# Kernel tuning notes

Hardware: AMD Instinct MI355X
Metric: run time of the kernel (lower is better)

The kernel has to match this reference:

```python
import jax, jax.numpy as jnp
import numpy as np
from jax import lax

DIL_R = 2            # dilation_radius
K = 2 * DIL_R + 1    # 5x5 morphology kernel
FOCAL_ALPHA = 0.25
FOCAL_GAMMA = 2.0
BOUNDARY_W = 1.0
IGNORE_IDX = 250


def setup_inputs() -> dict:
    key = jax.random.key(0)
    k1, k2 = jax.random.split(key)
    pred = jax.random.normal(k1, (32, 2, 512, 512), dtype=jnp.float32)
    target = jax.random.randint(k2, (32, 512, 512), 0, 2, dtype=jnp.int64)
    return {"pred": pred, "target": target}


def _boundary_mask(target):
    # labels float, 5x5 all-ones conv with 'same' padding (zero pad),
    # dilated = (conv > 0), eroded = (-conv(-x) > K*K-1) == (conv(x) > K*K-1)
    x = target.astype(jnp.float32)[:, None]                    # [B,1,H,W]
    kern = jnp.ones((1, 1, K, K), dtype=jnp.float32)
    s = lax.conv_general_dilated(x, kern, (1, 1), 'SAME',
                                 dimension_numbers=('NCHW', 'OIHW', 'NCHW'))
    dilated = (s > 0).astype(jnp.float32)
    eroded = (s > (K * K - 1)).astype(jnp.float32)
    return (dilated - eroded)[:, 0]                            # [B,H,W]


def _loss(pred, target, boundary):
    logp = jax.nn.log_softmax(pred, axis=1)                    # [B,2,H,W]
    # per-pixel CE
    ce_pix = -jnp.take_along_axis(logp, target[:, None].astype(jnp.int32), axis=1)[:, 0]  # [B,H,W]
    # main CE with ignore_index=250
    valid = (target != IGNORE_IDX)
    ce_loss = jnp.sum(ce_pix * valid) / jnp.maximum(jnp.sum(valid), 1)
    # focal loss (no ignore, mean over all pixels)
    pt = jnp.exp(-ce_pix)
    focal = jnp.mean(FOCAL_ALPHA * (1.0 - pt) ** FOCAL_GAMMA * ce_pix)
    # boundary dice on class-1 prob
    prob1 = jnp.exp(logp[:, 1])                                # softmax(pred,1)[:,1]
    tgt_f = target.astype(jnp.float32)
    bp = prob1 * boundary
    bt = tgt_f * boundary
    inter = jnp.sum(bp * bt, axis=(1, 2))
    union = jnp.sum(bp, axis=(1, 2)) + jnp.sum(bt, axis=(1, 2))
    dice = 2.0 * inter / (union + 1e-8)
    bdice = 1.0 - jnp.mean(dice)
    return ce_loss + BOUNDARY_W * focal + BOUNDARY_W * bdice


def reference(pred, target):
    boundary = _boundary_mask(target)
    return _loss(pred, target, boundary)
```

## Files before the change

kernel.cpp:

```cpp
#include <hip/hip_runtime.h>
#include <math.h>

#define BATCH 32
#define HH 512
#define WW 512
#define TH 16
#define HALO 2
#define SRH (TH + 2*HALO)
#define NDW (WW / 4)
#define CSTRIDE 132
#define NPIX ((float)BATCH * HH * WW)
#define HW (HH * WW)
#define NBLK (BATCH * (HH / TH))


__global__ __launch_bounds__(256, 4) void bel_main_kernel(
        const float* __restrict__ pred,
        const int*   __restrict__ target,
        float*       __restrict__ ws) {
    __shared__ unsigned int t8[SRH][NDW];
    __shared__ unsigned int csum[TH][CSTRIDE];
    __shared__ float red[6][4];

    const int tid = threadIdx.x;
    const int bid = blockIdx.x;
    const int b   = bid >> 5;
    const int ty  = bid & 31;
    const int y0  = ty * TH;
    const size_t tb = (size_t)b * HW;

    if (tid < 2 * TH) {
        int rr = tid >> 1;
        csum[rr][(tid & 1) ? (NDW + 1) : 0] = 0u;
    }

    #pragma unroll
    for (int it = 0; it < (SRH * NDW) / 256; ++it) {
        const int i  = tid + 256 * it;
        const int r  = i >> 7;
        const int c4 = i & 127;
        const int gy = y0 - HALO + r;
        unsigned int packed = 0u;
        if ((unsigned)gy < (unsigned)HH) {
            const int4 v = *(const int4*)(target + tb + ((size_t)gy << 9) + (c4 << 2));
            packed = (unsigned)v.x | ((unsigned)v.y << 8)
                   | ((unsigned)v.z << 16) | ((unsigned)v.w << 24);
        }
        t8[r][c4] = packed;
    }
    __syncthreads();

    #pragma unroll
    for (int it = 0; it < (TH * NDW) / 256; ++it) {
        const int j = tid + 256 * it;
        const int r = j >> 7;
        const int c = j & 127;
        csum[r][c + 1] = t8[r][c] + t8[r+1][c] + t8[r+2][c]
                       + t8[r+3][c] + t8[r+4][c];
    }
    __syncthreads();

    const float4* __restrict__ pr0 = (const float4*)(pred + tb * 2);
    const float4* __restrict__ pr1 = (const float4*)(pred + tb * 2 + HW);
    const int base4 = (y0 << 7) + tid;

    float4 F0[8], F1[8];
    #pragma unroll
    for (int it = 0; it < 8; ++it) F0[it] = pr0[base4 + 256 * it];
    #pragma unroll
    for (int it = 0; it < 8; ++it) F1[it] = pr1[base4 + 256 * it];

    float ce_acc = 0.f, cnt_acc = 0.f, focal_acc = 0.f;
    float inter_acc = 0.f, bp_acc = 0.f, bt_acc = 0.f;

    const unsigned long long M5 = 0xFFFFFFFFFFull;
    const unsigned long long ALL5 = 0x0505050505ull;

    const int g  = tid & 127;
    const int rb = tid >> 7;

    #pragma unroll
    for (int it = 0; it < 8; ++it) {
        const int r = rb + 2 * it;

        const float4 f0 = F0[it];
        const float4 f1 = F1[it];

        const unsigned int L = csum[r][g];
        const unsigned int M = csum[r][g + 1];
        const unsigned int R = csum[r][g + 2];
        const unsigned int tdw = t8[r + HALO][g];

        const unsigned long long lo  = (unsigned long long)L | ((unsigned long long)M << 32);
        const unsigned long long mid = (unsigned long long)M | ((unsigned long long)R << 32);

        #pragma unroll
        for (int i = 0; i < 4; ++i) {
            unsigned long long w;
            if      (i == 0) w = (lo  >> 16) & M5;
            else if (i == 1) w = (lo  >> 24) & M5;
            else if (i == 2) w =  mid        & M5;
            else             w = (mid >>  8) & M5;
            const float bm = (w != 0ull && w != ALL5) ? 1.0f : 0.0f;

            const unsigned int tv = (tdw >> (8 * i)) & 0xFFu;

            const float p0 = (i == 0) ? f0.x : (i == 1) ? f0.y : (i == 2) ? f0.z : f0.w;
            const float p1 = (i == 0) ? f1.x : (i == 1) ? f1.y : (i == 2) ? f1.z : f1.w;

            const float d  = p1 - p0;
            const float e  = __expf(-fabsf(d));
            const float rz = 1.0f / (1.0f + e);
            const float pmin = e * rz;
            const float prob1 = (d >= 0.0f) ? rz : pmin;
            const float pt = tv ? prob1 : (1.0f - prob1);
            const float ce = -__logf(pt);

            const float valid = (tv != 250u) ? 1.0f : 0.0f;
            ce_acc  += ce * valid;
            cnt_acc += valid;

            const float omp = 1.0f - pt;
            focal_acc += omp * omp * ce;

            const float bp = prob1 * bm;
            const float bt = (float)tv * bm;
            inter_acc += bp * bt;
            bp_acc    += bp;
            bt_acc    += bt;
        }
    }

    float vals[6] = {ce_acc, cnt_acc, focal_acc * 0.25f, inter_acc, bp_acc, bt_acc};
    #pragma unroll
    for (int jj = 0; jj < 6; ++jj) {
        float v = vals[jj];
        #pragma unroll
        for (int off = 32; off > 0; off >>= 1)
            v += __shfl_down(v, off, 64);
        vals[jj] = v;
    }
    const int wave = tid >> 6;
    const int lane = tid & 63;
    if (lane == 0) {
        #pragma unroll
        for (int jj = 0; jj < 6; ++jj) red[jj][wave] = vals[jj];
    }
    __syncthreads();
    if (tid == 0) {
        float* p = ws + bid * 8;
        #pragma unroll
        for (int jj = 0; jj < 6; ++jj)
            p[jj] = red[jj][0] + red[jj][1] + red[jj][2] + red[jj][3];
    }
}

__global__ void bel_finalize_kernel(const float* __restrict__ ws,
                                    float* __restrict__ out) {
    __shared__ float simg[BATCH][4];
    const int t = threadIdx.x;
    const int b = t >> 3;
    const int s = t & 7;

    float a0 = 0.f, a1 = 0.f, a2 = 0.f, a3 = 0.f, a4 = 0.f, a5 = 0.f;
    #pragma unroll
    for (int k = 0; k < 4; ++k) {
        const int bid = (b << 5) + s + (k << 3);
        const float* p = ws + bid * 8;
        a0 += p[0]; a1 += p[1]; a2 += p[2];
        a3 += p[3]; a4 += p[4]; a5 += p[5];
    }
    #pragma unroll
    for (int off = 4; off > 0; off >>= 1) {
        a0 += __shfl_down(a0, off, 8);
        a1 += __shfl_down(a1, off, 8);
        a2 += __shfl_down(a2, off, 8);
        a3 += __shfl_down(a3, off, 8);
        a4 += __shfl_down(a4, off, 8);
        a5 += __shfl_down(a5, off, 8);
    }
    if (s == 0) {
        simg[b][0] = a0;
        simg[b][1] = a1;
        simg[b][2] = a2;
        simg[b][3] = 2.0f * a3 / (a4 + a5 + 1e-8f);
    }
    __syncthreads();
    if (t < BATCH) {
        float ce  = simg[t][0];
        float cnt = simg[t][1];
        float foc = simg[t][2];
        float dc  = simg[t][3];
        #pragma unroll
        for (int off = 16; off > 0; off >>= 1) {
            ce  += __shfl_down(ce,  off, 32);
            cnt += __shfl_down(cnt, off, 32);
            foc += __shfl_down(foc, off, 32);
            dc  += __shfl_down(dc,  off, 32);
        }
        if (t == 0) {
            const float ce_loss = ce / fmaxf(cnt, 1.0f);
            const float focal   = foc / NPIX;
            const float bdice   = 1.0f - dc / (float)BATCH;
            out[0] = ce_loss + focal + bdice;
        }
    }
}

extern "C" void kernel_launch(void* const* d_in, const int* in_sizes, int n_in,
                              void* d_out, int out_size, void* d_ws, size_t ws_size,
                              hipStream_t stream) {
    const float* pred   = (const float*)d_in[0];
    const int*   target = (const int*)d_in[1];
    float* ws  = (float*)d_ws;
    float* out = (float*)d_out;

    bel_main_kernel<<<NBLK, 256, 0, stream>>>(pred, target, ws);
    bel_finalize_kernel<<<1, 256, 0, stream>>>(ws, out);
}
```

Baseline: 116.7 us.

## Split fused kernel into boundary-mask and loss kernels with finer grid

Splits the fused kernel in two. The first kernel computes the 5x5 boundary mask from the target labels and writes it as packed bytes to workspace. The second kernel streams pred, target and the mask across a finer grid of 2048 blocks to accumulate the loss partials. This drops the shared-memory staging and register-heavy preloading from the loss pass, which may raise occupancy, but it re-reads target, writes and reads an extra 8 MB mask, and adds a kernel launch.

```diff
diff --git a/kernel.cpp b/kernel.cpp
--- a/kernel.cpp
+++ b/kernel.cpp
@@ -11,16 +11,20 @@
 #define CSTRIDE 132
 #define NPIX ((float)BATCH * HH * WW)
 #define HW (HH * WW)
-#define NBLK (BATCH * (HH / TH))
-
-
-__global__ __launch_bounds__(256, 4) void bel_main_kernel(
-        const float* __restrict__ pred,
-        const int*   __restrict__ target,
-        float*       __restrict__ ws) {
+#define HW4 (HW / 4)
+#define NBLK_A (BATCH * (HH / TH))
+#define SEGS 64
+#define NBLK_B (BATCH * SEGS)
+#define NSTG ((SRH * NDW) / 256)
+#define NCS  ((TH * NDW) / 256)
+
+#define PARTIALS_FLOATS (NBLK_B * 8)
+
+__global__ __launch_bounds__(256) void boundary_kernel(
+        const int* __restrict__ target,
+        unsigned int* __restrict__ bmask) {
     __shared__ unsigned int t8[SRH][NDW];
     __shared__ unsigned int csum[TH][CSTRIDE];
-    __shared__ float red[6][4];
 
     const int tid = threadIdx.x;
     const int bid = blockIdx.x;
@@ -35,7 +39,7 @@
     }
 
     #pragma unroll
-    for (int it = 0; it < (SRH * NDW) / 256; ++it) {
+    for (int it = 0; it < NSTG; ++it) {
         const int i  = tid + 256 * it;
         const int r  = i >> 7;
         const int c4 = i & 127;
@@ -51,7 +55,7 @@
     __syncthreads();
 
     #pragma unroll
-    for (int it = 0; it < (TH * NDW) / 256; ++it) {
+    for (int it = 0; it < NCS; ++it) {
         const int j = tid + 256 * it;
         const int r = j >> 7;
         const int c = j & 127;
@@ -60,40 +64,23 @@
     }
     __syncthreads();
 
-    const float4* __restrict__ pr0 = (const float4*)(pred + tb * 2);
-    const float4* __restrict__ pr1 = (const float4*)(pred + tb * 2 + HW);
-    const int base4 = (y0 << 7) + tid;
-
-    float4 F0[8], F1[8];
-    #pragma unroll
-    for (int it = 0; it < 8; ++it) F0[it] = pr0[base4 + 256 * it];
-    #pragma unroll
-    for (int it = 0; it < 8; ++it) F1[it] = pr1[base4 + 256 * it];
-
-    float ce_acc = 0.f, cnt_acc = 0.f, focal_acc = 0.f;
-    float inter_acc = 0.f, bp_acc = 0.f, bt_acc = 0.f;
-
     const unsigned long long M5 = 0xFFFFFFFFFFull;
     const unsigned long long ALL5 = 0x0505050505ull;
-
     const int g  = tid & 127;
     const int rb = tid >> 7;
 
     #pragma unroll
     for (int it = 0; it < 8; ++it) {
         const int r = rb + 2 * it;
-
-        const float4 f0 = F0[it];
-        const float4 f1 = F1[it];
+        const int y = y0 + r;
 
         const unsigned int L = csum[r][g];
         const unsigned int M = csum[r][g + 1];
         const unsigned int R = csum[r][g + 2];
-        const unsigned int tdw = t8[r + HALO][g];
-
         const unsigned long long lo  = (unsigned long long)L | ((unsigned long long)M << 32);
         const unsigned long long mid = (unsigned long long)M | ((unsigned long long)R << 32);
 
+        unsigned int packed = 0u;
         #pragma unroll
         for (int i = 0; i < 4; ++i) {
             unsigned long long w;
@@ -101,22 +88,58 @@
             else if (i == 1) w = (lo  >> 24) & M5;
             else if (i == 2) w =  mid        & M5;
             else             w = (mid >>  8) & M5;
-            const float bm = (w != 0ull && w != ALL5) ? 1.0f : 0.0f;
-
-            const unsigned int tv = (tdw >> (8 * i)) & 0xFFu;
-
+            const unsigned int bm = (w != 0ull && w != ALL5) ? 1u : 0u;
+            packed |= bm << (8 * i);
+        }
+        bmask[(size_t)b * HW4 + (y << 7) + g] = packed;
+    }
+}
+
+__global__ __launch_bounds__(256) void loss_kernel(
+        const float* __restrict__ pred,
+        const int*   __restrict__ target,
+        const unsigned int* __restrict__ bmask,
+        float*       __restrict__ ws) {
+    __shared__ float red[6][4];
+
+    const int tid = threadIdx.x;
+    const int bid = blockIdx.x;
+    const int b   = bid >> 6;
+    const int seg = bid & 63;
+    const int base = (seg << 10) + tid;
+
+    const float4* __restrict__ p4 = (const float4*)pred;
+    const int4*   __restrict__ t4 = (const int4*)target;
+    const size_t pb = (size_t)b * (2 * HW4);
+    const size_t gb = (size_t)b * HW4;
+
+    float ce_acc = 0.f, cnt_acc = 0.f, focal_acc = 0.f;
+    float inter_acc = 0.f, bp_acc = 0.f, bt_acc = 0.f;
+
+    #pragma unroll
+    for (int k = 0; k < 4; ++k) {
+        const int hw4 = base + (k << 8);
+        const float4 f0 = p4[pb + hw4];
+        const float4 f1 = p4[pb + HW4 + hw4];
+        const int4   tv4 = t4[gb + hw4];
+        const unsigned int bm4 = bmask[gb + hw4];
+
+        #pragma unroll
+        for (int i = 0; i < 4; ++i) {
+            const int   t  = (i == 0) ? tv4.x : (i == 1) ? tv4.y : (i == 2) ? tv4.z : tv4.w;
             const float p0 = (i == 0) ? f0.x : (i == 1) ? f0.y : (i == 2) ? f0.z : f0.w;
             const float p1 = (i == 0) ? f1.x : (i == 1) ? f1.y : (i == 2) ? f1.z : f1.w;
+            const float bm = (float)((bm4 >> (8 * i)) & 1u);
 
             const float d  = p1 - p0;
             const float e  = __expf(-fabsf(d));
             const float rz = 1.0f / (1.0f + e);
             const float pmin = e * rz;
             const float prob1 = (d >= 0.0f) ? rz : pmin;
-            const float pt = tv ? prob1 : (1.0f - prob1);
+            const float pt = (t != 0) ? prob1 : (1.0f - prob1);
             const float ce = -__logf(pt);
 
-            const float valid = (tv != 250u) ? 1.0f : 0.0f;
+            const float valid = (t != 250) ? 1.0f : 0.0f;
             ce_acc  += ce * valid;
             cnt_acc += valid;
 
@@ -124,7 +147,7 @@
             focal_acc += omp * omp * ce;
 
             const float bp = prob1 * bm;
-            const float bt = (float)tv * bm;
+            const float bt = (float)t * bm;
             inter_acc += bp * bt;
             bp_acc    += bp;
             bt_acc    += bt;
@@ -164,8 +187,8 @@
 
     float a0 = 0.f, a1 = 0.f, a2 = 0.f, a3 = 0.f, a4 = 0.f, a5 = 0.f;
     #pragma unroll
-    for (int k = 0; k < 4; ++k) {
-        const int bid = (b << 5) + s + (k << 3);
+    for (int k = 0; k < SEGS / 8; ++k) {
+        const int bid = (b << 6) + (k << 3) + s;
         const float* p = ws + bid * 8;
         a0 += p[0]; a1 += p[1]; a2 += p[2];
         a3 += p[3]; a4 += p[4]; a5 += p[5];
@@ -188,18 +211,18 @@
     __syncthreads();
     if (t < BATCH) {
         float ce  = simg[t][0];
-        float cnt = simg[t][1];
+        float cn  = simg[t][1];
         float foc = simg[t][2];
         float dc  = simg[t][3];
         #pragma unroll
         for (int off = 16; off > 0; off >>= 1) {
             ce  += __shfl_down(ce,  off, 32);
-            cnt += __shfl_down(cnt, off, 32);
+            cn  += __shfl_down(cn,  off, 32);
             foc += __shfl_down(foc, off, 32);
             dc  += __shfl_down(dc,  off, 32);
         }
         if (t == 0) {
-            const float ce_loss = ce / fmaxf(cnt, 1.0f);
+            const float ce_loss = ce / fmaxf(cn, 1.0f);
             const float focal   = foc / NPIX;
             const float bdice   = 1.0f - dc / (float)BATCH;
             out[0] = ce_loss + focal + bdice;
@@ -214,7 +237,9 @@
     const int*   target = (const int*)d_in[1];
     float* ws  = (float*)d_ws;
     float* out = (float*)d_out;
-
-    bel_main_kernel<<<NBLK, 256, 0, stream>>>(pred, target, ws);
+    unsigned int* bmask = (unsigned int*)((char*)d_ws + 65536);
+
+    boundary_kernel<<<NBLK_A, 256, 0, stream>>>(target, bmask);
+    loss_kernel<<<NBLK_B, 256, 0, stream>>>(pred, target, bmask, ws);
     bel_finalize_kernel<<<1, 256, 0, stream>>>(ws, out);
 }
```

Result: slower. 124.1 us (+6.3%).
